# Kernel tuning notes

Measured on AMD Instinct MI355X. Metric: run time of the kernel, lower is better.

The kernel has to match this reference:

```python
import jax, jax.numpy as jnp
import numpy as np

N_USER = 100000
N_ITEM = 50000
D = 64
E_SOC = 3200000
E_INFO = 3200000
BATCH = 16384


def setup_inputs() -> dict:
    key = jax.random.key(0)
    ks = jax.random.split(key, 8)
    return {
        "user_emb": jax.random.normal(ks[0], (N_USER, D), dtype=jnp.float32) * 0.01,
        "item_emb": jax.random.normal(ks[1], (N_ITEM, D), dtype=jnp.float32) * 0.01,
        "social_rows": jax.random.randint(ks[2], (E_SOC,), 0, N_USER, dtype=jnp.int32),
        "social_cols": jax.random.randint(ks[3], (E_SOC,), 0, N_USER, dtype=jnp.int32),
        "social_vals": jnp.ones((E_SOC,), dtype=jnp.float32),
        "info_rows": jax.random.randint(ks[4], (E_INFO,), 0, N_USER, dtype=jnp.int32),
        "info_cols": jax.random.randint(ks[5], (E_INFO,), 0, N_ITEM, dtype=jnp.int32),
        "info_vals": jnp.ones((E_INFO,), dtype=jnp.float32),
        "user_ids": jax.random.randint(ks[6], (BATCH,), 0, N_USER, dtype=jnp.int32),
        "item_ids": jax.random.randint(ks[7], (BATCH,), 0, N_ITEM, dtype=jnp.int32),
    }


def _spmm(rows, cols, vals, feats, n_rows):
    # (A @ feats) where A is COO [n_rows, n_cols]: gather, weight, scatter-add.
    msgs = vals[:, None] * feats[cols]  # [E, D]
    return jax.ops.segment_sum(msgs, rows, num_segments=n_rows)


def reference(user_emb, item_emb, social_rows, social_cols, social_vals,
              info_rows, info_cols, info_vals, user_ids, item_ids):
    n_user = user_emb.shape[0]
    eps = 1e-8

    # user embedding from items: D_info^{-1} * info_adj @ item_emb
    deg_info = jax.ops.segment_sum(info_vals, info_rows, num_segments=n_user) + eps
    user_from_items = _spmm(info_rows, info_cols, info_vals, item_emb, n_user) / deg_info[:, None]

    # two GCN layers over social graph: H' = D^{-1} A H + H
    deg_soc = jax.ops.segment_sum(social_vals, social_rows, num_segments=n_user) + eps

    def gcn(h):
        return _spmm(social_rows, social_cols, social_vals, h, n_user) / deg_soc[:, None] + h

    h1 = gcn(user_emb)
    h2 = gcn(h1)
    final_user = h1 + h2 + user_from_items

    # final_item = item_emb + init_item_feature = 2 * item_emb
    final_item = 2.0 * item_emb

    u = final_user[user_ids]
    v = final_item[item_ids]
    return jax.nn.sigmoid(jnp.sum(u * v, axis=-1))
```

## Files before the change

kernel.cpp:

```cpp
#include <hip/hip_runtime.h>
#include <hip/hip_bf16.h>

#define BA 256
#define CHUNK_A 2048
#define PB 8
#define NBINS_MAX 512
#define CAPS 8800
#define PBM 4
#define NBINM_MAX 1024
#define CAPM_LDS 768

__device__ __forceinline__ float bf2f(unsigned short u) {
    return __uint_as_float(((unsigned int)u) << 16);
}
__device__ __forceinline__ unsigned short f2bf(float f) {
    unsigned int x = __float_as_uint(f);
    return (unsigned short)((x + 0x7fffu + ((x >> 16) & 1u)) >> 16);
}
__device__ __forceinline__ void unpk(unsigned int u, float& lo, float& hi) {
    lo = __uint_as_float(u << 16);
    hi = __uint_as_float(u & 0xffff0000u);
}
__device__ __forceinline__ unsigned int pack2(float lo, float hi) {
    return (unsigned int)f2bf(lo) | ((unsigned int)f2bf(hi) << 16);
}


__global__ __launch_bounds__(256) void conv_mark_kernel(const float* __restrict__ a,
                                                        unsigned short* __restrict__ oa, long long na,
                                                        const float* __restrict__ b,
                                                        unsigned short* __restrict__ ob, long long nb,
                                                        const int* __restrict__ ids,
                                                        int* __restrict__ mark,
                                                        int* __restrict__ mlist,
                                                        int* __restrict__ n_marked, int n,
                                                        int* __restrict__ curS, int nbinS, int capS,
                                                        int* __restrict__ curMI, int capM) {
    long long t = (long long)blockIdx.x * blockDim.x + threadIdx.x;
    long long i4 = t * 4;
    if (i4 < na) {
        float4 f = *(const float4*)&a[i4];
        ushort4 o = { f2bf(f.x), f2bf(f.y), f2bf(f.z), f2bf(f.w) };
        *(ushort4*)&oa[i4] = o;
    }
    if (i4 < nb) {
        float4 f = *(const float4*)&b[i4];
        ushort4 o = { f2bf(f.x), f2bf(f.y), f2bf(f.z), f2bf(f.w) };
        *(ushort4*)&ob[i4] = o;
    }
    int i = (int)t;
    if (i < nbinS) curS[i] = i * capS;
    if (i < NBINM_MAX) curMI[i] = i * capM;
    if (i < n) {
        int u = ids[i];
        if (atomicCAS(&mark[u], 0, -1) == 0) {
            int m = atomicAdd(n_marked, 1);
            mlist[m] = u;
            mark[u] = m + 1;
        }
    }
}

__global__ __launch_bounds__(256) void partA_all(const int* __restrict__ sr,
                                                 const int* __restrict__ sc,
                                                 const float* __restrict__ sv, int Es,
                                                 const int* __restrict__ ir,
                                                 const int* __restrict__ ic,
                                                 const float* __restrict__ iv, int Ei,
                                                 const int* __restrict__ mark,
                                                 int* __restrict__ curS, int2* __restrict__ bufS,
                                                 int nbinS, int capS,
                                                 int* __restrict__ curMI, int2* __restrict__ bufMI,
                                                 int capM) {
    __shared__ int hS[NBINS_MAX], gS[NBINS_MAX], lS[NBINS_MAX];
    __shared__ int hI[NBINM_MAX], gI[NBINM_MAX], lI[NBINM_MAX];
    int tid = threadIdx.x;
    int base = blockIdx.x * CHUNK_A;
    for (int b = tid; b < nbinS; b += BA) hS[b] = 0;
    for (int b = tid; b < NBINM_MAX; b += BA) hI[b] = 0;

    int e0 = base + tid * 8;
    int rS[8], cS[8], mI[8], cI[8];
    float vS[8], vI[8];
    int nS = (e0 < Es) ? min(8, Es - e0) : 0;
    int nI = (e0 < Ei) ? min(8, Ei - e0) : 0;
    if (nS == 8) {
        *(int4*)&rS[0] = *(const int4*)&sr[e0]; *(int4*)&rS[4] = *(const int4*)&sr[e0 + 4];
        *(int4*)&cS[0] = *(const int4*)&sc[e0]; *(int4*)&cS[4] = *(const int4*)&sc[e0 + 4];
        *(float4*)&vS[0] = *(const float4*)&sv[e0]; *(float4*)&vS[4] = *(const float4*)&sv[e0 + 4];
    } else {
        #pragma unroll 8
        for (int k = 0; k < 8; ++k)
            if (k < nS) { rS[k] = sr[e0 + k]; cS[k] = sc[e0 + k]; vS[k] = sv[e0 + k]; }
    }
    int rI[8];
    if (nI == 8) {
        *(int4*)&rI[0] = *(const int4*)&ir[e0]; *(int4*)&rI[4] = *(const int4*)&ir[e0 + 4];
        *(int4*)&cI[0] = *(const int4*)&ic[e0]; *(int4*)&cI[4] = *(const int4*)&ic[e0 + 4];
        *(float4*)&vI[0] = *(const float4*)&iv[e0]; *(float4*)&vI[4] = *(const float4*)&iv[e0 + 4];
    } else {
        #pragma unroll 8
        for (int k = 0; k < 8; ++k)
            if (k < nI) { rI[k] = ir[e0 + k]; cI[k] = ic[e0 + k]; vI[k] = iv[e0 + k]; }
    }
    #pragma unroll 8
    for (int k = 0; k < 8; ++k) mI[k] = (k < nI) ? mark[rI[k]] : 0;
    __syncthreads();

    #pragma unroll 8
    for (int k = 0; k < 8; ++k) if (k < nS) atomicAdd(&hS[rS[k] >> PB], 1);
    #pragma unroll 8
    for (int k = 0; k < 8; ++k) if (mI[k] > 0) atomicAdd(&hI[(mI[k] - 1) >> PBM], 1);
    __syncthreads();

    for (int b = tid; b < nbinS; b += BA) {
        int h = hS[b]; gS[b] = h ? atomicAdd(&curS[b], h) : 0; lS[b] = 0;
    }
    for (int b = tid; b < NBINM_MAX; b += BA) {
        int h = hI[b]; gI[b] = h ? atomicAdd(&curMI[b], h) : 0; lI[b] = 0;
    }
    __syncthreads();

    #pragma unroll 8
    for (int k = 0; k < 8; ++k) {
        if (k < nS) {
            int r = rS[k];
            int b = r >> PB;
            int off = atomicAdd(&lS[b], 1);
            long long dst = (long long)gS[b] + off;
            if (dst < (long long)(b + 1) * capS)
                bufS[dst] = make_int2(((r & 255) << 17) | cS[k], __float_as_int(vS[k]));
        }
    }
    #pragma unroll 8
    for (int k = 0; k < 8; ++k) {
        if (mI[k] > 0) {
            int m = mI[k] - 1;
            int b = m >> PBM;
            int off = atomicAdd(&lI[b], 1);
            long long dst = (long long)gI[b] + off;
            if (dst < (long long)(b + 1) * capM)
                bufMI[dst] = make_int2(((m & 15) << 17) | cI[k], __float_as_int(vI[k]));
        }
    }
}

__global__ __launch_bounds__(512) void partB_sort(const int* __restrict__ curS,
                                                  const int2* __restrict__ bufS,
                                                  int2* __restrict__ csr,
                                                  int2* __restrict__ rowptr2,
                                                  int n_user, int capS) {
    int bin = blockIdx.x;
    int rows0 = bin << PB;
    int nrows = min(256, n_user - rows0);
    __shared__ int cur[256], wsum[4];
    int tid = threadIdx.x;
    if (tid < 256) cur[tid] = 0;
    __syncthreads();
    int gstart = bin * capS;
    int gend = curS[bin];
    if (gend > gstart + capS) gend = gstart + capS;
    int cnt = gend - gstart;
    for (int i = tid; i < cnt; i += 512) atomicAdd(&cur[bufS[gstart + i].x >> 17], 1);
    __syncthreads();
    int lane = tid & 63, wid = tid >> 6;
    int x = 0, v = 0;
    if (tid < 256) {
        x = cur[tid]; v = x;
        #pragma unroll
        for (int d = 1; d < 64; d <<= 1) { int y = __shfl_up(v, d); if (lane >= d) v += y; }
        if (lane == 63) wsum[wid] = v;
    }
    __syncthreads();
    if (tid == 0) {
        int s = 0;
        #pragma unroll
        for (int k = 0; k < 4; ++k) { int t = wsum[k]; wsum[k] = s; s += t; }
    }
    __syncthreads();
    if (tid < 256) {
        int excl = wsum[wid] + v - x;
        if (tid < nrows) rowptr2[rows0 + tid] = make_int2(gstart + excl, gstart + excl + x);
        cur[tid] = excl;
    }
    __syncthreads();
    for (int i = tid; i < cnt; i += 512) {
        int2 e = bufS[gstart + i];
        int rl = e.x >> 17;
        int p = atomicAdd(&cur[rl], 1);
        csr[gstart + p] = make_int2(e.x & 0x1FFFF, e.y);
    }
}

__global__ __launch_bounds__(256) void gather1_kernel(const int2* __restrict__ rowptr2,
                                                      const int2* __restrict__ csr,
                                                      const unsigned short* __restrict__ ub,
                                                      unsigned short* __restrict__ hb,
                                                      int n_user) {
    int w = (int)((blockIdx.x * (long long)blockDim.x + threadIdx.x) >> 6);
    if (w >= n_user) return;
    int lane = threadIdx.x & 63;
    int sub = lane >> 3;
    int d8 = (lane & 7) << 3;
    int2 seg = rowptr2[w];
    float a0 = 0, a1 = 0, a2 = 0, a3 = 0, a4 = 0, a5 = 0, a6 = 0, a7 = 0, degs = 0;
    for (int j = seg.x + sub; j < seg.y; j += 8) {
        int2 e = csr[j];
        float vv = __int_as_float(e.y);
        int4 q = *(const int4*)&ub[(long long)e.x * 64 + d8];
        float f0, f1, f2, f3, f4, f5, f6, f7;
        unpk(q.x, f0, f1); unpk(q.y, f2, f3); unpk(q.z, f4, f5); unpk(q.w, f6, f7);
        a0 += vv * f0; a1 += vv * f1; a2 += vv * f2; a3 += vv * f3;
        a4 += vv * f4; a5 += vv * f5; a6 += vv * f6; a7 += vv * f7;
        degs += vv;
    }
    #pragma unroll
    for (int m = 8; m < 64; m <<= 1) {
        a0 += __shfl_xor(a0, m); a1 += __shfl_xor(a1, m);
        a2 += __shfl_xor(a2, m); a3 += __shfl_xor(a3, m);
        a4 += __shfl_xor(a4, m); a5 += __shfl_xor(a5, m);
        a6 += __shfl_xor(a6, m); a7 += __shfl_xor(a7, m);
        degs += __shfl_xor(degs, m);
    }
    if (sub == 0) {
        float inv = 1.0f / (degs + 1e-8f);
        int4 qe = *(const int4*)&ub[(long long)w * 64 + d8];
        float g0, g1, g2, g3, g4, g5, g6, g7;
        unpk(qe.x, g0, g1); unpk(qe.y, g2, g3); unpk(qe.z, g4, g5); unpk(qe.w, g6, g7);
        int4 o;
        o.x = (int)pack2(fmaf(a0, inv, g0), fmaf(a1, inv, g1));
        o.y = (int)pack2(fmaf(a2, inv, g2), fmaf(a3, inv, g3));
        o.z = (int)pack2(fmaf(a4, inv, g4), fmaf(a5, inv, g5));
        o.w = (int)pack2(fmaf(a6, inv, g6), fmaf(a7, inv, g7));
        *(int4*)&hb[(long long)w * 64 + d8] = o;
    }
}

__global__ __launch_bounds__(256) void accS_kernel(const int* __restrict__ mlist,
                                                   const int* __restrict__ n_marked,
                                                   const int2* __restrict__ rowptr2,
                                                   const int2* __restrict__ csr,
                                                   const unsigned short* __restrict__ hb,
                                                   float* __restrict__ accS) {
    int w = (int)((blockIdx.x * (long long)blockDim.x + threadIdx.x) >> 6);
    if (w >= *n_marked) return;
    int lane = threadIdx.x & 63;
    int sub = lane >> 3;
    int d8 = (lane & 7) << 3;
    int r = mlist[w];
    int2 seg = rowptr2[r];
    float a0 = 0, a1 = 0, a2 = 0, a3 = 0, a4 = 0, a5 = 0, a6 = 0, a7 = 0, degs = 0;
    for (int j = seg.x + sub; j < seg.y; j += 8) {
        int2 e = csr[j];
        float vv = __int_as_float(e.y);
        int4 q = *(const int4*)&hb[(long long)e.x * 64 + d8];
        float f0, f1, f2, f3, f4, f5, f6, f7;
        unpk(q.x, f0, f1); unpk(q.y, f2, f3); unpk(q.z, f4, f5); unpk(q.w, f6, f7);
        a0 += vv * f0; a1 += vv * f1; a2 += vv * f2; a3 += vv * f3;
        a4 += vv * f4; a5 += vv * f5; a6 += vv * f6; a7 += vv * f7;
        degs += vv;
    }
    #pragma unroll
    for (int m = 8; m < 64; m <<= 1) {
        a0 += __shfl_xor(a0, m); a1 += __shfl_xor(a1, m);
        a2 += __shfl_xor(a2, m); a3 += __shfl_xor(a3, m);
        a4 += __shfl_xor(a4, m); a5 += __shfl_xor(a5, m);
        a6 += __shfl_xor(a6, m); a7 += __shfl_xor(a7, m);
        degs += __shfl_xor(degs, m);
    }
    if (sub == 0) {
        float inv = 1.0f / (degs + 1e-8f);
        long long base = (long long)w * 64 + d8;
        float4 o0 = { a0 * inv, a1 * inv, a2 * inv, a3 * inv };
        float4 o1 = { a4 * inv, a5 * inv, a6 * inv, a7 * inv };
        *(float4*)&accS[base] = o0;
        *(float4*)&accS[base + 4] = o1;
    }
}

__global__ __launch_bounds__(256) void partB_accI(const int* __restrict__ n_marked,
                                                  const int* __restrict__ curMI,
                                                  const int2* __restrict__ bufMI,
                                                  const unsigned short* __restrict__ ib,
                                                  float* __restrict__ accI, int capM) {
    int bin = blockIdx.x;
    int nm = *n_marked;
    int rows0 = bin << PBM;
    if (rows0 >= nm) return;
    int nrows = min(16, nm - rows0);
    __shared__ int2 sI[CAPM_LDS];
    __shared__ int j0[17], cI[16];
    int tid = threadIdx.x;
    if (tid < 16) cI[tid] = 0;
    __syncthreads();
    long long gs = (long long)bin * capM;
    long long ge = curMI[bin];
    if (ge > gs + capM) ge = gs + capM;
    int cnt = (int)(ge - gs);
    for (int i = tid; i < cnt; i += 256) atomicAdd(&cI[bufMI[gs + i].x >> 17], 1);
    __syncthreads();
    int lane = tid & 63, wid = tid >> 6;
    if (wid == 0 && lane < 16) {
        int x = cI[lane], v = x;
        #pragma unroll
        for (int d = 1; d < 16; d <<= 1) { int y = __shfl_up(v, d); if (lane >= d) v += y; }
        j0[lane] = v - x; cI[lane] = v - x;
        if (lane == 15) j0[16] = v;
    }
    __syncthreads();
    for (int i = tid; i < cnt; i += 256) {
        int2 e = bufMI[gs + i];
        int p = atomicAdd(&cI[e.x >> 17], 1);
        sI[p] = make_int2(e.x & 0x1FFFF, e.y);
    }
    __syncthreads();
    int sub = lane >> 4, d4 = (lane & 15) << 2;
    for (int r = wid; r < nrows; r += 4) {
        int a = j0[r], b2 = j0[r + 1];
        float4 acc = make_float4(0.f, 0.f, 0.f, 0.f);
        float degs = 0.f;
        for (int j = a + sub; j < b2; j += 4) {
            int2 e = sI[j];
            float vv = __int_as_float(e.y);
            ushort4 q = *(const ushort4*)&ib[(long long)e.x * 64 + d4];
            acc.x += vv * bf2f(q.x); acc.y += vv * bf2f(q.y);
            acc.z += vv * bf2f(q.z); acc.w += vv * bf2f(q.w);
            degs += vv;
        }
        #pragma unroll
        for (int m = 16; m < 64; m <<= 1) {
            acc.x += __shfl_xor(acc.x, m); acc.y += __shfl_xor(acc.y, m);
            acc.z += __shfl_xor(acc.z, m); acc.w += __shfl_xor(acc.w, m);
            degs  += __shfl_xor(degs, m);
        }
        if (sub == 0) {
            float inv = 1.0f / (degs + 1e-8f);
            float4 o = make_float4(acc.x * inv, acc.y * inv, acc.z * inv, acc.w * inv);
            *(float4*)&accI[(long long)(rows0 + r) * 64 + d4] = o;
        }
    }
}

__global__ __launch_bounds__(256) void dot_kernel(const unsigned short* __restrict__ hb,
                                                  const float* __restrict__ accS,
                                                  const float* __restrict__ accI,
                                                  const unsigned short* __restrict__ ib,
                                                  const int* __restrict__ mark,
                                                  const int* __restrict__ uids,
                                                  const int* __restrict__ iids,
                                                  float* __restrict__ out, int batch) {
    int w = (int)((blockIdx.x * (long long)blockDim.x + threadIdx.x) >> 6);
    int lane = threadIdx.x & 63;
    if (w >= batch) return;
    int u = uids[w], it = iids[w];
    long long m = (long long)(mark[u] - 1);
    float uv = 2.0f * bf2f(hb[(long long)u * 64 + lane]) + accS[m * 64 + lane] + accI[m * 64 + lane];
    float vv = 2.0f * bf2f(ib[(long long)it * 64 + lane]);
    float p = uv * vv;
    #pragma unroll
    for (int off = 32; off; off >>= 1) p += __shfl_xor(p, off);
    if (lane == 0) out[w] = 1.0f / (1.0f + __expf(-p));
}


extern "C" void kernel_launch(void* const* d_in, const int* in_sizes, int n_in,
                              void* d_out, int out_size, void* d_ws, size_t ws_size,
                              hipStream_t stream) {
    const float* user_emb  = (const float*)d_in[0];
    const float* item_emb  = (const float*)d_in[1];
    const int*   soc_rows  = (const int*)d_in[2];
    const int*   soc_cols  = (const int*)d_in[3];
    const float* soc_vals  = (const float*)d_in[4];
    const int*   info_rows = (const int*)d_in[5];
    const int*   info_cols = (const int*)d_in[6];
    const float* info_vals = (const float*)d_in[7];
    const int*   user_ids  = (const int*)d_in[8];
    const int*   item_ids  = (const int*)d_in[9];
    float*       out       = (float*)d_out;

    const int n_user = in_sizes[0] / 64;
    const int n_item = in_sizes[1] / 64;
    const int E_soc  = in_sizes[2];
    const int E_info = in_sizes[5];
    const int batch  = in_sizes[8];

    const int nbinS = (n_user + 255) >> PB;
    int capS = (int)((long long)E_soc * 256 / n_user);
    capS = capS + capS / 16 + 96;
    if (capS > CAPS) capS = CAPS;
    int capM = (int)((long long)E_info * 16 / n_user);
    capM = capM + capM / 4 + 64;
    if (capM > CAPM_LDS) capM = CAPM_LDS;

    char* p = (char*)d_ws;
    auto alloc = [&](size_t bytes) { char* q = p; p += (bytes + 255) & ~size_t(255); return q; };
    int* mark     = (int*)alloc(sizeof(int) * n_user);
    int* n_marked = (int*)alloc(sizeof(int) * 64);
    size_t zero_bytes = (size_t)(p - (char*)d_ws);
    int*  mlist   = (int*)alloc(sizeof(int) * batch);
    int*  curSoc  = (int*)alloc(sizeof(int) * nbinS);
    int*  curMI   = (int*)alloc(sizeof(int) * NBINM_MAX);
    int2* bufSoc  = (int2*)alloc(sizeof(int2) * (size_t)nbinS * capS);
    int2* csrSoc  = (int2*)alloc(sizeof(int2) * (size_t)nbinS * capS);
    int2* rowptr2 = (int2*)alloc(sizeof(int2) * (size_t)n_user);
    int2* bufMI   = (int2*)alloc(sizeof(int2) * (size_t)NBINM_MAX * capM);
    unsigned short* ub = (unsigned short*)alloc(sizeof(short) * (size_t)n_user * 64);
    unsigned short* ib = (unsigned short*)alloc(sizeof(short) * (size_t)n_item * 64);
    unsigned short* hb = (unsigned short*)alloc(sizeof(short) * (size_t)n_user * 64);
    float* accS        = (float*)alloc(sizeof(float) * (size_t)batch * 64);
    float* accI        = (float*)alloc(sizeof(float) * (size_t)batch * 64);
    (void)ws_size;

    hipMemsetAsync(d_ws, 0, zero_bytes, stream);

    const int B = 256;
    long long na = (long long)n_user * 64, nbm = (long long)n_item * 64;
    long long c4 = (na > nbm ? na : nbm) / 4;
    conv_mark_kernel<<<(int)((c4 + B - 1) / B), B, 0, stream>>>(
        user_emb, ub, na, item_emb, ib, nbm,
        user_ids, mark, mlist, n_marked, batch,
        curSoc, nbinS, capS, curMI, capM);

    int Emax = max(E_soc, E_info);
    int gA = (Emax + CHUNK_A - 1) / CHUNK_A;
    partA_all<<<gA, BA, 0, stream>>>(soc_rows, soc_cols, soc_vals, E_soc,
                                     info_rows, info_cols, info_vals, E_info,
                                     mark, curSoc, bufSoc, nbinS, capS,
                                     curMI, bufMI, capM);

    partB_sort<<<nbinS, 512, 0, stream>>>(curSoc, bufSoc, csrSoc, rowptr2, n_user, capS);

    long long t1 = (long long)n_user * 64;
    gather1_kernel<<<(int)((t1 + B - 1) / B), B, 0, stream>>>(rowptr2, csrSoc, ub, hb, n_user);

    long long t2 = (long long)batch * 64;
    accS_kernel<<<(int)((t2 + B - 1) / B), B, 0, stream>>>(mlist, n_marked, rowptr2, csrSoc,
                                                           hb, accS);

    int gBi = (batch + 15) >> PBM;
    partB_accI<<<gBi, B, 0, stream>>>(n_marked, curMI, bufMI, ib, accI, capM);

    dot_kernel<<<(int)((t2 + B - 1) / B), B, 0, stream>>>(hb, accS, accI, ib, mark,
                                                          user_ids, item_ids, out, batch);
}
```

Before: 217.3 us.

## Bucket info edges into 256-row bins, reuse partB_sort, fuse item aggregation into accS

The info-graph edges for marked users now go into 64 bins of 256 rows each, using the social capacity, instead of 1024 bins of 16. A second partB_sort launch builds a CSR for them, and the separate partB_accI kernel is removed. The item aggregation is folded into the accS kernel as accSI, which writes one combined accumulator that dot_kernel reads. partA is widened to 512 threads per block covering 4096 edges, and one fewer fp32 buffer round-trips through memory. In exchange it adds a sort launch and more atomic contention on fewer bin counters in partA.

```diff
diff --git a/kernel.cpp b/kernel.cpp
--- a/kernel.cpp
+++ b/kernel.cpp
@@ -1,14 +1,12 @@
 #include <hip/hip_runtime.h>
 #include <hip/hip_bf16.h>
 
-#define BA 256
-#define CHUNK_A 2048
+#define BA 512
+#define CHUNK_A 4096
 #define PB 8
 #define NBINS_MAX 512
 #define CAPS 8800
-#define PBM 4
-#define NBINM_MAX 1024
-#define CAPM_LDS 768
+#define NBINM_C 64
 
 __device__ __forceinline__ float bf2f(unsigned short u) {
     return __uint_as_float(((unsigned int)u) << 16);
@@ -34,8 +32,8 @@
                                                         int* __restrict__ mark,
                                                         int* __restrict__ mlist,
                                                         int* __restrict__ n_marked, int n,
-                                                        int* __restrict__ curS, int nbinS, int capS,
-                                                        int* __restrict__ curMI, int capM) {
+                                                        int* __restrict__ curS, int nbinS,
+                                                        int* __restrict__ curMI, int capS) {
     long long t = (long long)blockIdx.x * blockDim.x + threadIdx.x;
     long long i4 = t * 4;
     if (i4 < na) {
@@ -50,7 +48,7 @@
     }
     int i = (int)t;
     if (i < nbinS) curS[i] = i * capS;
-    if (i < NBINM_MAX) curMI[i] = i * capM;
+    if (i < NBINM_C) curMI[i] = i * capS;
     if (i < n) {
         int u = ids[i];
         if (atomicCAS(&mark[u], 0, -1) == 0) {
@@ -61,7 +59,7 @@
     }
 }
 
-__global__ __launch_bounds__(256) void partA_all(const int* __restrict__ sr,
+__global__ __launch_bounds__(512) void partA_all(const int* __restrict__ sr,
                                                  const int* __restrict__ sc,
                                                  const float* __restrict__ sv, int Es,
                                                  const int* __restrict__ ir,
@@ -70,14 +68,13 @@
                                                  const int* __restrict__ mark,
                                                  int* __restrict__ curS, int2* __restrict__ bufS,
                                                  int nbinS, int capS,
-                                                 int* __restrict__ curMI, int2* __restrict__ bufMI,
-                                                 int capM) {
+                                                 int* __restrict__ curMI, int2* __restrict__ bufMI) {
     __shared__ int hS[NBINS_MAX], gS[NBINS_MAX], lS[NBINS_MAX];
-    __shared__ int hI[NBINM_MAX], gI[NBINM_MAX], lI[NBINM_MAX];
+    __shared__ int hI[NBINM_C], gI[NBINM_C], lI[NBINM_C];
     int tid = threadIdx.x;
     int base = blockIdx.x * CHUNK_A;
     for (int b = tid; b < nbinS; b += BA) hS[b] = 0;
-    for (int b = tid; b < NBINM_MAX; b += BA) hI[b] = 0;
+    if (tid < NBINM_C) hI[tid] = 0;
 
     int e0 = base + tid * 8;
     int rS[8], cS[8], mI[8], cI[8];
@@ -110,14 +107,14 @@
     #pragma unroll 8
     for (int k = 0; k < 8; ++k) if (k < nS) atomicAdd(&hS[rS[k] >> PB], 1);
     #pragma unroll 8
-    for (int k = 0; k < 8; ++k) if (mI[k] > 0) atomicAdd(&hI[(mI[k] - 1) >> PBM], 1);
+    for (int k = 0; k < 8; ++k) if (mI[k] > 0) atomicAdd(&hI[(mI[k] - 1) >> 8], 1);
     __syncthreads();
 
     for (int b = tid; b < nbinS; b += BA) {
         int h = hS[b]; gS[b] = h ? atomicAdd(&curS[b], h) : 0; lS[b] = 0;
     }
-    for (int b = tid; b < NBINM_MAX; b += BA) {
-        int h = hI[b]; gI[b] = h ? atomicAdd(&curMI[b], h) : 0; lI[b] = 0;
+    if (tid < NBINM_C) {
+        int h = hI[tid]; gI[tid] = h ? atomicAdd(&curMI[tid], h) : 0; lI[tid] = 0;
     }
     __syncthreads();
 
@@ -136,32 +133,32 @@
     for (int k = 0; k < 8; ++k) {
         if (mI[k] > 0) {
             int m = mI[k] - 1;
-            int b = m >> PBM;
+            int b = m >> 8;
             int off = atomicAdd(&lI[b], 1);
             long long dst = (long long)gI[b] + off;
-            if (dst < (long long)(b + 1) * capM)
-                bufMI[dst] = make_int2(((m & 15) << 17) | cI[k], __float_as_int(vI[k]));
+            if (dst < (long long)(b + 1) * capS)
+                bufMI[dst] = make_int2(((m & 255) << 17) | cI[k], __float_as_int(vI[k]));
         }
     }
 }
 
-__global__ __launch_bounds__(512) void partB_sort(const int* __restrict__ curS,
-                                                  const int2* __restrict__ bufS,
+__global__ __launch_bounds__(512) void partB_sort(const int* __restrict__ cur_in,
+                                                  const int2* __restrict__ buf,
                                                   int2* __restrict__ csr,
                                                   int2* __restrict__ rowptr2,
-                                                  int n_user, int capS) {
+                                                  int n_rows_total, int cap) {
     int bin = blockIdx.x;
-    int rows0 = bin << PB;
-    int nrows = min(256, n_user - rows0);
+    int rows0 = bin << 8;
+    int nrows = min(256, n_rows_total - rows0);
     __shared__ int cur[256], wsum[4];
     int tid = threadIdx.x;
     if (tid < 256) cur[tid] = 0;
     __syncthreads();
-    int gstart = bin * capS;
-    int gend = curS[bin];
-    if (gend > gstart + capS) gend = gstart + capS;
+    int gstart = bin * cap;
+    int gend = cur_in[bin];
+    if (gend > gstart + cap) gend = gstart + cap;
     int cnt = gend - gstart;
-    for (int i = tid; i < cnt; i += 512) atomicAdd(&cur[bufS[gstart + i].x >> 17], 1);
+    for (int i = tid; i < cnt; i += 512) atomicAdd(&cur[buf[gstart + i].x >> 17], 1);
     __syncthreads();
     int lane = tid & 63, wid = tid >> 6;
     int x = 0, v = 0;
@@ -185,7 +182,7 @@
     }
     __syncthreads();
     for (int i = tid; i < cnt; i += 512) {
-        int2 e = bufS[gstart + i];
+        int2 e = buf[gstart + i];
         int rl = e.x >> 17;
         int p = atomicAdd(&cur[rl], 1);
         csr[gstart + p] = make_int2(e.x & 0x1FFFF, e.y);
@@ -236,29 +233,45 @@
     }
 }
 
-__global__ __launch_bounds__(256) void accS_kernel(const int* __restrict__ mlist,
-                                                   const int* __restrict__ n_marked,
-                                                   const int2* __restrict__ rowptr2,
-                                                   const int2* __restrict__ csr,
-                                                   const unsigned short* __restrict__ hb,
-                                                   float* __restrict__ accS) {
+__global__ __launch_bounds__(256) void accSI_kernel(const int* __restrict__ mlist,
+                                                    const int* __restrict__ n_marked,
+                                                    const int2* __restrict__ rowptr2,
+                                                    const int2* __restrict__ csrS,
+                                                    const unsigned short* __restrict__ hb,
+                                                    const int2* __restrict__ rowptrI2,
+                                                    const int2* __restrict__ csrI,
+                                                    const unsigned short* __restrict__ ib,
+                                                    float* __restrict__ accF) {
     int w = (int)((blockIdx.x * (long long)blockDim.x + threadIdx.x) >> 6);
     if (w >= *n_marked) return;
     int lane = threadIdx.x & 63;
     int sub = lane >> 3;
     int d8 = (lane & 7) << 3;
     int r = mlist[w];
+
+    float a0 = 0, a1 = 0, a2 = 0, a3 = 0, a4 = 0, a5 = 0, a6 = 0, a7 = 0, dS = 0;
     int2 seg = rowptr2[r];
-    float a0 = 0, a1 = 0, a2 = 0, a3 = 0, a4 = 0, a5 = 0, a6 = 0, a7 = 0, degs = 0;
     for (int j = seg.x + sub; j < seg.y; j += 8) {
-        int2 e = csr[j];
+        int2 e = csrS[j];
         float vv = __int_as_float(e.y);
         int4 q = *(const int4*)&hb[(long long)e.x * 64 + d8];
         float f0, f1, f2, f3, f4, f5, f6, f7;
         unpk(q.x, f0, f1); unpk(q.y, f2, f3); unpk(q.z, f4, f5); unpk(q.w, f6, f7);
         a0 += vv * f0; a1 += vv * f1; a2 += vv * f2; a3 += vv * f3;
         a4 += vv * f4; a5 += vv * f5; a6 += vv * f6; a7 += vv * f7;
-        degs += vv;
+        dS += vv;
+    }
+    float b0 = 0, b1 = 0, b2 = 0, b3 = 0, b4 = 0, b5 = 0, b6 = 0, b7 = 0, dI = 0;
+    seg = rowptrI2[w];
+    for (int j = seg.x + sub; j < seg.y; j += 8) {
+        int2 e = csrI[j];
+        float vv = __int_as_float(e.y);
+        int4 q = *(const int4*)&ib[(long long)e.x * 64 + d8];
+        float f0, f1, f2, f3, f4, f5, f6, f7;
+        unpk(q.x, f0, f1); unpk(q.y, f2, f3); unpk(q.z, f4, f5); unpk(q.w, f6, f7);
+        b0 += vv * f0; b1 += vv * f1; b2 += vv * f2; b3 += vv * f3;
+        b4 += vv * f4; b5 += vv * f5; b6 += vv * f6; b7 += vv * f7;
+        dI += vv;
     }
     #pragma unroll
     for (int m = 8; m < 64; m <<= 1) {
@@ -266,84 +279,26 @@
         a2 += __shfl_xor(a2, m); a3 += __shfl_xor(a3, m);
         a4 += __shfl_xor(a4, m); a5 += __shfl_xor(a5, m);
         a6 += __shfl_xor(a6, m); a7 += __shfl_xor(a7, m);
-        degs += __shfl_xor(degs, m);
+        dS += __shfl_xor(dS, m);
+        b0 += __shfl_xor(b0, m); b1 += __shfl_xor(b1, m);
+        b2 += __shfl_xor(b2, m); b3 += __shfl_xor(b3, m);
+        b4 += __shfl_xor(b4, m); b5 += __shfl_xor(b5, m);
+        b6 += __shfl_xor(b6, m); b7 += __shfl_xor(b7, m);
+        dI += __shfl_xor(dI, m);
     }
     if (sub == 0) {
-        float inv = 1.0f / (degs + 1e-8f);
+        float iS = 1.0f / (dS + 1e-8f);
+        float iI = 1.0f / (dI + 1e-8f);
         long long base = (long long)w * 64 + d8;
-        float4 o0 = { a0 * inv, a1 * inv, a2 * inv, a3 * inv };
-        float4 o1 = { a4 * inv, a5 * inv, a6 * inv, a7 * inv };
-        *(float4*)&accS[base] = o0;
-        *(float4*)&accS[base + 4] = o1;
-    }
-}
-
-__global__ __launch_bounds__(256) void partB_accI(const int* __restrict__ n_marked,
-                                                  const int* __restrict__ curMI,
-                                                  const int2* __restrict__ bufMI,
-                                                  const unsigned short* __restrict__ ib,
-                                                  float* __restrict__ accI, int capM) {
-    int bin = blockIdx.x;
-    int nm = *n_marked;
-    int rows0 = bin << PBM;
-    if (rows0 >= nm) return;
-    int nrows = min(16, nm - rows0);
-    __shared__ int2 sI[CAPM_LDS];
-    __shared__ int j0[17], cI[16];
-    int tid = threadIdx.x;
-    if (tid < 16) cI[tid] = 0;
-    __syncthreads();
-    long long gs = (long long)bin * capM;
-    long long ge = curMI[bin];
-    if (ge > gs + capM) ge = gs + capM;
-    int cnt = (int)(ge - gs);
-    for (int i = tid; i < cnt; i += 256) atomicAdd(&cI[bufMI[gs + i].x >> 17], 1);
-    __syncthreads();
-    int lane = tid & 63, wid = tid >> 6;
-    if (wid == 0 && lane < 16) {
-        int x = cI[lane], v = x;
-        #pragma unroll
-        for (int d = 1; d < 16; d <<= 1) { int y = __shfl_up(v, d); if (lane >= d) v += y; }
-        j0[lane] = v - x; cI[lane] = v - x;
-        if (lane == 15) j0[16] = v;
-    }
-    __syncthreads();
-    for (int i = tid; i < cnt; i += 256) {
-        int2 e = bufMI[gs + i];
-        int p = atomicAdd(&cI[e.x >> 17], 1);
-        sI[p] = make_int2(e.x & 0x1FFFF, e.y);
-    }
-    __syncthreads();
-    int sub = lane >> 4, d4 = (lane & 15) << 2;
-    for (int r = wid; r < nrows; r += 4) {
-        int a = j0[r], b2 = j0[r + 1];
-        float4 acc = make_float4(0.f, 0.f, 0.f, 0.f);
-        float degs = 0.f;
-        for (int j = a + sub; j < b2; j += 4) {
-            int2 e = sI[j];
-            float vv = __int_as_float(e.y);
-            ushort4 q = *(const ushort4*)&ib[(long long)e.x * 64 + d4];
-            acc.x += vv * bf2f(q.x); acc.y += vv * bf2f(q.y);
-            acc.z += vv * bf2f(q.z); acc.w += vv * bf2f(q.w);
-            degs += vv;
-        }
-        #pragma unroll
-        for (int m = 16; m < 64; m <<= 1) {
-            acc.x += __shfl_xor(acc.x, m); acc.y += __shfl_xor(acc.y, m);
-            acc.z += __shfl_xor(acc.z, m); acc.w += __shfl_xor(acc.w, m);
-            degs  += __shfl_xor(degs, m);
-        }
-        if (sub == 0) {
-            float inv = 1.0f / (degs + 1e-8f);
-            float4 o = make_float4(acc.x * inv, acc.y * inv, acc.z * inv, acc.w * inv);
-            *(float4*)&accI[(long long)(rows0 + r) * 64 + d4] = o;
-        }
+        float4 o0 = { a0 * iS + b0 * iI, a1 * iS + b1 * iI, a2 * iS + b2 * iI, a3 * iS + b3 * iI };
+        float4 o1 = { a4 * iS + b4 * iI, a5 * iS + b5 * iI, a6 * iS + b6 * iI, a7 * iS + b7 * iI };
+        *(float4*)&accF[base] = o0;
+        *(float4*)&accF[base + 4] = o1;
     }
 }
 
 __global__ __launch_bounds__(256) void dot_kernel(const unsigned short* __restrict__ hb,
-                                                  const float* __restrict__ accS,
-                                                  const float* __restrict__ accI,
+                                                  const float* __restrict__ accF,
                                                   const unsigned short* __restrict__ ib,
                                                   const int* __restrict__ mark,
                                                   const int* __restrict__ uids,
@@ -354,7 +309,7 @@
     if (w >= batch) return;
     int u = uids[w], it = iids[w];
     long long m = (long long)(mark[u] - 1);
-    float uv = 2.0f * bf2f(hb[(long long)u * 64 + lane]) + accS[m * 64 + lane] + accI[m * 64 + lane];
+    float uv = 2.0f * bf2f(hb[(long long)u * 64 + lane]) + accF[m * 64 + lane];
     float vv = 2.0f * bf2f(ib[(long long)it * 64 + lane]);
     float p = uv * vv;
     #pragma unroll
@@ -385,30 +340,29 @@
     const int batch  = in_sizes[8];
 
     const int nbinS = (n_user + 255) >> PB;
+    const int nbinM = (batch + 255) >> 8;
     int capS = (int)((long long)E_soc * 256 / n_user);
     capS = capS + capS / 16 + 96;
     if (capS > CAPS) capS = CAPS;
-    int capM = (int)((long long)E_info * 16 / n_user);
-    capM = capM + capM / 4 + 64;
-    if (capM > CAPM_LDS) capM = CAPM_LDS;
 
     char* p = (char*)d_ws;
     auto alloc = [&](size_t bytes) { char* q = p; p += (bytes + 255) & ~size_t(255); return q; };
     int* mark     = (int*)alloc(sizeof(int) * n_user);
     int* n_marked = (int*)alloc(sizeof(int) * 64);
     size_t zero_bytes = (size_t)(p - (char*)d_ws);
-    int*  mlist   = (int*)alloc(sizeof(int) * batch);
-    int*  curSoc  = (int*)alloc(sizeof(int) * nbinS);
-    int*  curMI   = (int*)alloc(sizeof(int) * NBINM_MAX);
-    int2* bufSoc  = (int2*)alloc(sizeof(int2) * (size_t)nbinS * capS);
-    int2* csrSoc  = (int2*)alloc(sizeof(int2) * (size_t)nbinS * capS);
-    int2* rowptr2 = (int2*)alloc(sizeof(int2) * (size_t)n_user);
-    int2* bufMI   = (int2*)alloc(sizeof(int2) * (size_t)NBINM_MAX * capM);
+    int*  mlist    = (int*)alloc(sizeof(int) * batch);
+    int*  curSoc   = (int*)alloc(sizeof(int) * nbinS);
+    int*  curMI    = (int*)alloc(sizeof(int) * NBINM_C);
+    int2* bufSoc   = (int2*)alloc(sizeof(int2) * (size_t)nbinS * capS);
+    int2* csrSoc   = (int2*)alloc(sizeof(int2) * (size_t)nbinS * capS);
+    int2* rowptr2  = (int2*)alloc(sizeof(int2) * (size_t)n_user);
+    int2* bufMI    = (int2*)alloc(sizeof(int2) * (size_t)nbinM * capS);
+    int2* csrI     = (int2*)alloc(sizeof(int2) * (size_t)nbinM * capS);
+    int2* rowptrI2 = (int2*)alloc(sizeof(int2) * (size_t)batch);
     unsigned short* ub = (unsigned short*)alloc(sizeof(short) * (size_t)n_user * 64);
     unsigned short* ib = (unsigned short*)alloc(sizeof(short) * (size_t)n_item * 64);
     unsigned short* hb = (unsigned short*)alloc(sizeof(short) * (size_t)n_user * 64);
-    float* accS        = (float*)alloc(sizeof(float) * (size_t)batch * 64);
-    float* accI        = (float*)alloc(sizeof(float) * (size_t)batch * 64);
+    float* accF        = (float*)alloc(sizeof(float) * (size_t)batch * 64);
     (void)ws_size;
 
     hipMemsetAsync(d_ws, 0, zero_bytes, stream);
@@ -419,27 +373,26 @@
     conv_mark_kernel<<<(int)((c4 + B - 1) / B), B, 0, stream>>>(
         user_emb, ub, na, item_emb, ib, nbm,
         user_ids, mark, mlist, n_marked, batch,
-        curSoc, nbinS, capS, curMI, capM);
+        curSoc, nbinS, curMI, capS);
 
     int Emax = max(E_soc, E_info);
     int gA = (Emax + CHUNK_A - 1) / CHUNK_A;
     partA_all<<<gA, BA, 0, stream>>>(soc_rows, soc_cols, soc_vals, E_soc,
                                      info_rows, info_cols, info_vals, E_info,
                                      mark, curSoc, bufSoc, nbinS, capS,
-                                     curMI, bufMI, capM);
+                                     curMI, bufMI);
 
     partB_sort<<<nbinS, 512, 0, stream>>>(curSoc, bufSoc, csrSoc, rowptr2, n_user, capS);
+    partB_sort<<<nbinM, 512, 0, stream>>>(curMI, bufMI, csrI, rowptrI2, batch, capS);
 
     long long t1 = (long long)n_user * 64;
     gather1_kernel<<<(int)((t1 + B - 1) / B), B, 0, stream>>>(rowptr2, csrSoc, ub, hb, n_user);
 
     long long t2 = (long long)batch * 64;
-    accS_kernel<<<(int)((t2 + B - 1) / B), B, 0, stream>>>(mlist, n_marked, rowptr2, csrSoc,
-                                                           hb, accS);
-
-    int gBi = (batch + 15) >> PBM;
-    partB_accI<<<gBi, B, 0, stream>>>(n_marked, curMI, bufMI, ib, accI, capM);
-
-    dot_kernel<<<(int)((t2 + B - 1) / B), B, 0, stream>>>(hb, accS, accI, ib, mark,
+    accSI_kernel<<<(int)((t2 + B - 1) / B), B, 0, stream>>>(mlist, n_marked,
+                                                            rowptr2, csrSoc, hb,
+                                                            rowptrI2, csrI, ib, accF);
+
+    dot_kernel<<<(int)((t2 + B - 1) / B), B, 0, stream>>>(hb, accF, ib, mark,
                                                           user_ids, item_ids, out, batch);
 }
```

Result: faster. 207.5 us (-4.5%).
